# Kernel optimization log

Hardware: AMD Instinct MI355X
Metric: run time of the kernel (lower is better)

## Reference

```python
import jax, jax.numpy as jnp
import numpy as np

B, CI, CO, H, W = 16, 32, 32, 256, 256
K0, K1 = 32, 32              # modes_fourier
LEVEL0, LEVEL1 = 3, 5        # PDEPara_mode_level
M = 2 ** LEVEL1              # 32 = modes_pde_extra per dim
KAPPA = (2 * M) // (2 ** LEVEL0)  # 8 = kappa_base
NPARA = 3 * (LEVEL0 - 1) + 1      # 7 columns of fourierweight_scaling used


def setup_inputs() -> dict:
    key = jax.random.key(0)
    ks = jax.random.split(key, 6)
    scale = 1.0 / (CI * CO)
    x = jax.random.normal(ks[0], (B, CI, H, W), dtype=jnp.float32)
    fourierweight_scaling = jax.random.uniform(ks[1], (B, NPARA), dtype=jnp.float32)
    weights_dim0 = scale * jax.random.uniform(ks[2], (CI, CO, K0, K1, 2), dtype=jnp.float32)
    weights_dim1 = scale * jax.random.uniform(ks[3], (CI, CO, K0, K1, 2), dtype=jnp.float32)
    weights_extra_dim0 = scale * jax.random.uniform(ks[4], (CI, CO, M, M, 2), dtype=jnp.float32)
    weights_extra_dim1 = scale * jax.random.uniform(ks[5], (CI, CO, M, M, 2), dtype=jnp.float32)
    return dict(x=x, fourierweight_scaling=fourierweight_scaling,
                weights_dim0=weights_dim0, weights_dim1=weights_dim1,
                weights_extra_dim0=weights_extra_dim0, weights_extra_dim1=weights_extra_dim1)


def _c(w):
    # real-pair [..., 2] -> complex; compl2/compl3_einsum are exactly complex products
    return jax.lax.complex(w[..., 0], w[..., 1])


def _mode_scaling(fs):
    # hierarchical quadrant-wise per-mode scaling, [B, M, M]
    s = jnp.zeros((B, M, M), dtype=fs.dtype)
    s = s.at[:, :KAPPA, :KAPPA].set(fs[:, 0][:, None, None])
    for d in range(1, LEVEL0):  # small fixed number of levels
        l0 = KAPPA * 2 ** (d - 1)
        l1 = 2 * l0
        s = s.at[:, :l0, l0:l1].set(fs[:, 3 * d - 2][:, None, None])
        s = s.at[:, l0:l1, :l0].set(fs[:, 3 * d - 1][:, None, None])
        s = s.at[:, l0:l1, l0:l1].set(fs[:, 3 * d][:, None, None])
    return s


def reference(x, fourierweight_scaling, weights_dim0, weights_dim1,
              weights_extra_dim0, weights_extra_dim1):
    x_ft = jnp.fft.rfft2(x, norm='ortho')  # [B, CI, H, W//2+1] complex
    out_ft = jnp.zeros((B, CO, H, W // 2 + 1), dtype=x_ft.dtype)
    # base mode mixing on low / high row-frequency corners
    out_ft = out_ft.at[:, :, :K0, :K1].set(
        jnp.einsum('bixy,ioxy->boxy', x_ft[:, :, :K0, :K1], _c(weights_dim0)))
    out_ft = out_ft.at[:, :, -K0:, :K1].set(
        jnp.einsum('bixy,ioxy->boxy', x_ft[:, :, -K0:, :K1], _c(weights_dim1)))
    # PDE-parameter dependent extra mixing with hierarchical scaling
    s = _mode_scaling(fourierweight_scaling).astype(x_ft.dtype)
    out_ft = out_ft.at[:, :, :M, :M].add(
        jnp.einsum('bixy,ioxy,bxy->boxy', x_ft[:, :, :M, :M], _c(weights_extra_dim0), s))
    out_ft = out_ft.at[:, :, -M:, :M].add(
        jnp.einsum('bixy,ioxy,bxy->boxy', x_ft[:, :, -M:, :M], _c(weights_extra_dim1), s))
    return jnp.fft.irfft2(out_ft, s=(H, W), norm='ortho')  # [B, CO, H, W]
```

## Files before the change

kernel.cpp:

```cpp
#include <hip/hip_runtime.h>


typedef _Float16 f16;
typedef _Float16 f16x8 __attribute__((ext_vector_type(8)));
typedef float f32x4 __attribute__((ext_vector_type(4)));

static __device__ __forceinline__ float2 upk(uint u) {
    union { uint x; f16 h[2]; } c; c.x = u;
    return make_float2((float)c.h[0], (float)c.h[1]);
}
static __device__ __forceinline__ uint pk2(float r, float i) {
    union { uint x; f16 h[2]; } c; c.h[0] = (f16)r; c.h[1] = (f16)i;
    return c.x;
}

__global__ void k_tabs(f16* __restrict__ Etab, f16* __restrict__ Ftabt,
                       f16* __restrict__ Etab2, f16* __restrict__ Tt) {
    const int h = blockIdx.x;
    const int tid = threadIdx.x;
    if (tid < 64) {
        const int j = tid;
        const int ky = (j < 32) ? j : j - 64;
        float s, c;
        sincospif((float)(ky * h) / 128.0f, &s, &c);
        Etab[h * 128 + 2 * j] = (f16)c;
        Etab[h * 128 + 2 * j + 1] = (f16)s;
        Etab2[j * 512 + 2 * h] = (f16)c;
        Etab2[j * 512 + 2 * h + 1] = (f16)s;
    } else if (tid < 96) {
        const int k = tid - 64;
        const float ck = (k == 0) ? 1.0f : 2.0f;
        float s, c;
        sincospif((float)(k * h) / 128.0f, &s, &c);
        Ftabt[h * 64 + 2 * k] = (f16)(ck * c);
        Ftabt[h * 64 + 2 * k + 1] = (f16)(-ck * s);
    } else {
        const int kx = tid - 96;
        float s, c;
        sincospif((float)(kx * h) / 128.0f, &s, &c);
        Tt[(2 * kx) * 256 + h] = (f16)c;
        Tt[(2 * kx + 1) * 256 + h] = (f16)(-s);
    }
}

__global__ __launch_bounds__(256) void k_rowdftB(const float* __restrict__ x,
                                                 const f16* __restrict__ Tt,
                                                 f16* __restrict__ Xw16) {
    __shared__ __align__(16) f16 Gs[128 * 88];
    const int tid = threadIdx.x;
    const int wv = tid >> 6, lane = tid & 63;
    const int l15 = lane & 15, lk = lane >> 4;
    const long rowbase = (long)blockIdx.x * 128;

    f32x4 acc[2][4];
#pragma unroll
    for (int mt = 0; mt < 2; ++mt)
#pragma unroll
        for (int nt = 0; nt < 4; ++nt)
            acc[mt][nt] = (f32x4){0.0f, 0.0f, 0.0f, 0.0f};

    const float* xbase = x + (rowbase + wv * 32 + l15) * 256 + lk * 8;
    const f16* tbase = Tt + l15 * 256 + lk * 8;

#pragma unroll
    for (int ks = 0; ks < 8; ++ks) {
        f16x8 a[2], b[4];
#pragma unroll
        for (int mt = 0; mt < 2; ++mt) {
            const float4 u = *(const float4*)(xbase + mt * 4096 + ks * 32);
            const float4 v = *(const float4*)(xbase + mt * 4096 + ks * 32 + 4);
            a[mt][0] = (f16)u.x; a[mt][1] = (f16)u.y;
            a[mt][2] = (f16)u.z; a[mt][3] = (f16)u.w;
            a[mt][4] = (f16)v.x; a[mt][5] = (f16)v.y;
            a[mt][6] = (f16)v.z; a[mt][7] = (f16)v.w;
        }
#pragma unroll
        for (int nt = 0; nt < 4; ++nt)
            b[nt] = *(const f16x8*)(tbase + nt * 4096 + ks * 32);
#pragma unroll
        for (int mt = 0; mt < 2; ++mt)
#pragma unroll
            for (int nt = 0; nt < 4; ++nt)
                acc[mt][nt] = __builtin_amdgcn_mfma_f32_16x16x32_f16(
                    a[mt], b[nt], acc[mt][nt], 0, 0, 0);
    }

#pragma unroll
    for (int mt = 0; mt < 2; ++mt)
#pragma unroll
        for (int nt = 0; nt < 4; ++nt) {
            const int row0 = wv * 32 + mt * 16 + lk * 4;
            const int col = nt * 16 + l15;
#pragma unroll
            for (int r = 0; r < 4; ++r)
                Gs[(row0 + r) * 88 + col] = (f16)acc[mt][nt][r];
        }
    __syncthreads();

#pragma unroll
    for (int p = 0; p < 4; ++p) {
        const int id = p * 256 + tid;
        const int row = id >> 3, ch = id & 7;
        *(uint4*)(Xw16 + (rowbase + row) * 64 + ch * 8) =
            *(const uint4*)(Gs + row * 88 + ch * 8);
    }
}

__global__ __launch_bounds__(256) void k_coldftB(const f16* __restrict__ Xw16,
                                                 const f16* __restrict__ Etab2,
                                                 f16* __restrict__ Xf16) {
    __shared__ __align__(16) f16 Bt[64 * 520];
    const int tid = threadIdx.x;
    const long p = blockIdx.x;

    {
        const uint* src = (const uint*)(Xw16 + (p * 256 + tid) * 64);
        uint* B32 = (uint*)Bt;
#pragma unroll
        for (int kx = 0; kx < 32; ++kx) {
            const uint a = src[kx];
            const uint b = (a >> 16) | (((a & 0xffffu) ^ 0x8000u) << 16);
            B32[(2 * kx) * 260 + tid] = a;
            B32[(2 * kx + 1) * 260 + tid] = b;
        }
    }
    __syncthreads();

    const int wv = tid >> 6, lane = tid & 63;
    const int l15 = lane & 15, lk = lane >> 4;

    f32x4 acc[4];
#pragma unroll
    for (int nt = 0; nt < 4; ++nt) acc[nt] = (f32x4){0.0f, 0.0f, 0.0f, 0.0f};

    const f16* abase = Etab2 + (wv * 16 + l15) * 512 + lk * 8;
#pragma unroll
    for (int ks = 0; ks < 16; ++ks) {
        const f16x8 a = *(const f16x8*)(abase + ks * 32);
        f16x8 b[4];
#pragma unroll
        for (int nt = 0; nt < 4; ++nt)
            b[nt] = *(const f16x8*)(Bt + (nt * 16 + l15) * 520 + ks * 32 + lk * 8);
#pragma unroll
        for (int nt = 0; nt < 4; ++nt)
            acc[nt] = __builtin_amdgcn_mfma_f32_16x16x32_f16(a, b[nt], acc[nt], 0, 0, 0);
    }

    f16* obase = Xf16 + p * 4096;
#pragma unroll
    for (int nt = 0; nt < 4; ++nt)
#pragma unroll
        for (int r = 0; r < 4; ++r)
            obase[(wv * 16 + lk * 4 + r) * 64 + nt * 16 + l15] = (f16)acc[nt][r];
}

__global__ __launch_bounds__(256) void k_mixB(const f16* __restrict__ Xf16,
                                              const float* __restrict__ fs,
                                              const float* __restrict__ w0,
                                              const float* __restrict__ w1,
                                              const float* __restrict__ we0,
                                              const float* __restrict__ we1,
                                              f16* __restrict__ Ff16) {
    __shared__ __align__(16) float4 Wl[4096];
    const int tid = threadIdx.x;
    const int bid = blockIdx.x;
    const int cog = bid >> 6;
    const int corner = (bid >> 5) & 1;
    const int jj = bid & 31;
    const int j = corner * 32 + jj;

    {
        const int t = tid >> 7, ci = (tid >> 2) & 31, co = tid & 3;
        const float* Wt = (t == 0) ? (corner ? w1 : w0) : (corner ? we1 : we0);
        const float4* src =
            (const float4*)(Wt + ((long)(ci * 32 + cog * 4 + co) * 2048 + jj * 64));
        const int m = tid & 15;
#pragma unroll
        for (int i = 0; i < 16; ++i) Wl[tid * 16 + (i ^ m)] = src[i];
    }
    __syncthreads();

    const int b = tid >> 4, kxp = tid & 15;
    const int kx0 = 2 * kxp;

    float s[2];
#pragma unroll
    for (int e = 0; e < 2; ++e) {
        const int v = kx0 + e, u = jj;
        int idx;
        if (u < 8 && v < 8) idx = 0;
        else if (u < 16 && v < 16) idx = (u < 8) ? 1 : ((v < 8) ? 2 : 3);
        else idx = (u < 16) ? 4 : ((v < 16) ? 5 : 6);
        s[e] = fs[b * 7 + idx];
    }

    float aW[4][4] = {}, aE[4][4] = {};
    const uint* xb = (const uint*)Xf16 + (long)(b * 32) * 2048 + j * 32 + kx0;

    for (int ci = 0; ci < 32; ++ci) {
        const uint2 xu = *(const uint2*)(xb + ci * 2048);
        const float2 x0 = upk(xu.x), x1 = upk(xu.y);
        const int rbase = ci * 4;
#pragma unroll
        for (int co = 0; co < 4; ++co) {
            const int rw = rbase + co;
            const int sl = kxp ^ (rw & 15);
            const float4 wv = Wl[rw * 16 + sl];
            const float4 ev = Wl[(128 + rw) * 16 + sl];
            aW[co][0] += x0.x * wv.x - x0.y * wv.y;
            aW[co][1] += x0.x * wv.y + x0.y * wv.x;
            aW[co][2] += x1.x * wv.z - x1.y * wv.w;
            aW[co][3] += x1.x * wv.w + x1.y * wv.z;
            aE[co][0] += x0.x * ev.x - x0.y * ev.y;
            aE[co][1] += x0.x * ev.y + x0.y * ev.x;
            aE[co][2] += x1.x * ev.z - x1.y * ev.w;
            aE[co][3] += x1.x * ev.w + x1.y * ev.z;
        }
    }

    uint* ofb = (uint*)Ff16;
#pragma unroll
    for (int co = 0; co < 4; ++co) {
        const long q = b * 32 + cog * 4 + co;
        uint2 o;
        o.x = pk2(aW[co][0] + s[0] * aE[co][0], aW[co][1] + s[0] * aE[co][1]);
        o.y = pk2(aW[co][2] + s[1] * aE[co][2], aW[co][3] + s[1] * aE[co][3]);
        *(uint2*)(ofb + q * 2048 + j * 32 + kx0) = o;
    }
}

__global__ __launch_bounds__(256) void k_invB(const f16* __restrict__ Ff16,
                                              const f16* __restrict__ Etab,
                                              f16* __restrict__ Gbuf) {
    __shared__ __align__(16) f16 Ft[64 * 136];
    __shared__ __align__(16) f16 Gs[256 * 72];
    const int tid = threadIdx.x;
    const long q = blockIdx.x;

    {
        const uint4* src = (const uint4*)(Ff16 + q * 4096);
        uint* B32 = (uint*)Ft;
#pragma unroll
        for (int i = 0; i < 2; ++i) {
            const uint4 v = src[tid * 2 + i];
            const uint a4[4] = {v.x, v.y, v.z, v.w};
#pragma unroll
            for (int c = 0; c < 4; ++c) {
                const int idx = tid * 8 + i * 4 + c;
                const int jr = idx >> 5, kx = idx & 31;
                const uint a = a4[c];
                B32[(2 * kx) * 68 + jr] = a ^ 0x80000000u;
                B32[(2 * kx + 1) * 68 + jr] = (a >> 16) | (a << 16);
            }
        }
    }
    __syncthreads();

    const int wv = tid >> 6, lane = tid & 63;
    const int l15 = lane & 15, lk = lane >> 4;

    f32x4 acc[4][4];
#pragma unroll
    for (int mt = 0; mt < 4; ++mt)
#pragma unroll
        for (int nt = 0; nt < 4; ++nt)
            acc[mt][nt] = (f32x4){0.0f, 0.0f, 0.0f, 0.0f};

    const f16* Arow = Etab + (wv * 64 + l15) * 128 + lk * 8;
#pragma unroll
    for (int ks = 0; ks < 4; ++ks) {
        f16x8 a[4], b[4];
#pragma unroll
        for (int mt = 0; mt < 4; ++mt)
            a[mt] = *(const f16x8*)(Arow + mt * 2048 + ks * 32);
#pragma unroll
        for (int nt = 0; nt < 4; ++nt)
            b[nt] = *(const f16x8*)(&Ft[(nt * 16 + l15) * 136 + ks * 32 + lk * 8]);
#pragma unroll
        for (int mt = 0; mt < 4; ++mt)
#pragma unroll
            for (int nt = 0; nt < 4; ++nt)
                acc[mt][nt] = __builtin_amdgcn_mfma_f32_16x16x32_f16(
                    a[mt], b[nt], acc[mt][nt], 0, 0, 0);
    }

#pragma unroll
    for (int mt = 0; mt < 4; ++mt)
#pragma unroll
        for (int nt = 0; nt < 4; ++nt) {
            const int row = wv * 64 + mt * 16 + lk * 4;
            const int col = nt * 16 + l15;
#pragma unroll
            for (int r = 0; r < 4; ++r)
                Gs[(row + r) * 72 + col] = (f16)acc[mt][nt][r];
        }
    __syncthreads();

#pragma unroll
    for (int p = 0; p < 8; ++p) {
        const int id = p * 256 + tid;
        const int row = id >> 3, ch = id & 7;
        const uint4 u = *(const uint4*)(Gs + row * 72 + ch * 8);
        *(uint4*)(Gbuf + q * 16384 + row * 64 + ch * 8) = u;
    }
}

__global__ __launch_bounds__(256) void k_invC(const f16* __restrict__ Gbuf,
                                              const f16* __restrict__ Ftabt,
                                              float* __restrict__ out) {
    const int tid = threadIdx.x;
    const long q = blockIdx.x >> 1;
    const int half = blockIdx.x & 1;
    const int wv = tid >> 6, lane = tid & 63;
    const int l15 = lane & 15, lk = lane >> 4;

    f16x8 a[2][2];
    const f16* abase = Gbuf + q * 16384 + (half * 128 + wv * 32 + l15) * 64 + lk * 8;
#pragma unroll
    for (int mt = 0; mt < 2; ++mt)
#pragma unroll
        for (int ks = 0; ks < 2; ++ks)
            a[mt][ks] = *(const f16x8*)(abase + mt * 1024 + ks * 32);

    float* obase = out + q * 65536 + (long)(half * 128 + wv * 32) * 256;

#pragma unroll 1
    for (int g = 0; g < 4; ++g) {
        f32x4 acc[2][4];
#pragma unroll
        for (int mt = 0; mt < 2; ++mt)
#pragma unroll
            for (int nt = 0; nt < 4; ++nt)
                acc[mt][nt] = (f32x4){0.0f, 0.0f, 0.0f, 0.0f};

        const f16* bbase = Ftabt + (g * 64 + l15) * 64 + lk * 8;
#pragma unroll
        for (int nt = 0; nt < 4; ++nt)
#pragma unroll
            for (int ks = 0; ks < 2; ++ks) {
                const f16x8 b = *(const f16x8*)(bbase + nt * 1024 + ks * 32);
#pragma unroll
                for (int mt = 0; mt < 2; ++mt)
                    acc[mt][nt] = __builtin_amdgcn_mfma_f32_16x16x32_f16(
                        a[mt][ks], b, acc[mt][nt], 0, 0, 0);
            }

#pragma unroll
        for (int mt = 0; mt < 2; ++mt)
#pragma unroll
            for (int nt = 0; nt < 4; ++nt) {
                float* o = obase + (mt * 16 + lk * 4) * 256 + g * 64 + nt * 16 + l15;
#pragma unroll
                for (int r = 0; r < 4; ++r)
                    o[r * 256] = acc[mt][nt][r] * 0x1p-16f;
            }
    }
}

extern "C" void kernel_launch(void* const* d_in, const int* in_sizes, int n_in,
                              void* d_out, int out_size, void* d_ws, size_t ws_size,
                              hipStream_t stream) {
    (void)in_sizes; (void)n_in; (void)out_size; (void)ws_size;
    const float* x   = (const float*)d_in[0];
    const float* fs  = (const float*)d_in[1];
    const float* w0  = (const float*)d_in[2];
    const float* w1  = (const float*)d_in[3];
    const float* we0 = (const float*)d_in[4];
    const float* we1 = (const float*)d_in[5];
    float* out = (float*)d_out;
    float* ws = (float*)d_ws;

    f16* Etab   = (f16*)ws;
    f16* Ftabt  = (f16*)(ws + 16384);
    f16* Etab2  = (f16*)(ws + 24576);
    f16* Tt     = (f16*)(ws + 40960);
    f16* Xw16   = (f16*)(ws + 49152);
    f16* Gbuf   = (f16*)(ws + 49152 + 4194304);
    f16* Xf16   = (f16*)(ws + 49152 + 8388608);
    f16* Ff16   = (f16*)(ws + 49152 + 8388608 + 2097152);

    k_tabs   <<<256,  128, 0, stream>>>(Etab, Ftabt, Etab2, Tt);
    k_rowdftB<<<1024, 256, 0, stream>>>(x, Tt, Xw16);
    k_coldftB<<<512,  256, 0, stream>>>(Xw16, Etab2, Xf16);
    k_mixB   <<<512,  256, 0, stream>>>(Xf16, fs, w0, w1, we0, we1, Ff16);
    k_invB   <<<512,  256, 0, stream>>>(Ff16, Etab, Gbuf);
    k_invC   <<<1024, 256, 0, stream>>>(Gbuf, Ftabt, out);
}
```

Measured before the change: 319.7 us.

## Fuse row and column DFT stages and the two inverse stages into single kernels

Merges the forward row DFT and column DFT into one kernel that keeps the intermediate in LDS instead of writing it to global memory. The split real/imag layout of Etab2 and the sign-flipped copy are built directly from the MFMA accumulators. Likewise merges the two inverse stages so the intermediate G stays in LDS, cutting two global round trips and two launches. Each block now does more work with larger accumulator tiles, which raises register pressure and reduces parallelism in the final stage (512 blocks instead of 1024).

```diff
diff --git a/kernel.cpp b/kernel.cpp
--- a/kernel.cpp
+++ b/kernel.cpp
@@ -25,8 +25,8 @@
         sincospif((float)(ky * h) / 128.0f, &s, &c);
         Etab[h * 128 + 2 * j] = (f16)c;
         Etab[h * 128 + 2 * j + 1] = (f16)s;
-        Etab2[j * 512 + 2 * h] = (f16)c;
-        Etab2[j * 512 + 2 * h + 1] = (f16)s;
+        Etab2[j * 512 + h] = (f16)c;
+        Etab2[j * 512 + 256 + h] = (f16)s;
     } else if (tid < 96) {
         const int k = tid - 64;
         const float ck = (k == 0) ? 1.0f : 2.0f;
@@ -43,115 +43,92 @@
     }
 }
 
-__global__ __launch_bounds__(256) void k_rowdftB(const float* __restrict__ x,
-                                                 const f16* __restrict__ Tt,
-                                                 f16* __restrict__ Xw16) {
-    __shared__ __align__(16) f16 Gs[128 * 88];
-    const int tid = threadIdx.x;
-    const int wv = tid >> 6, lane = tid & 63;
-    const int l15 = lane & 15, lk = lane >> 4;
-    const long rowbase = (long)blockIdx.x * 128;
-
-    f32x4 acc[2][4];
-#pragma unroll
-    for (int mt = 0; mt < 2; ++mt)
-#pragma unroll
-        for (int nt = 0; nt < 4; ++nt)
-            acc[mt][nt] = (f32x4){0.0f, 0.0f, 0.0f, 0.0f};
-
-    const float* xbase = x + (rowbase + wv * 32 + l15) * 256 + lk * 8;
-    const f16* tbase = Tt + l15 * 256 + lk * 8;
-
-#pragma unroll
-    for (int ks = 0; ks < 8; ++ks) {
-        f16x8 a[2], b[4];
-#pragma unroll
-        for (int mt = 0; mt < 2; ++mt) {
-            const float4 u = *(const float4*)(xbase + mt * 4096 + ks * 32);
-            const float4 v = *(const float4*)(xbase + mt * 4096 + ks * 32 + 4);
-            a[mt][0] = (f16)u.x; a[mt][1] = (f16)u.y;
-            a[mt][2] = (f16)u.z; a[mt][3] = (f16)u.w;
-            a[mt][4] = (f16)v.x; a[mt][5] = (f16)v.y;
-            a[mt][6] = (f16)v.z; a[mt][7] = (f16)v.w;
-        }
-#pragma unroll
-        for (int nt = 0; nt < 4; ++nt)
-            b[nt] = *(const f16x8*)(tbase + nt * 4096 + ks * 32);
-#pragma unroll
-        for (int mt = 0; mt < 2; ++mt)
-#pragma unroll
-            for (int nt = 0; nt < 4; ++nt)
-                acc[mt][nt] = __builtin_amdgcn_mfma_f32_16x16x32_f16(
-                    a[mt], b[nt], acc[mt][nt], 0, 0, 0);
-    }
-
-#pragma unroll
-    for (int mt = 0; mt < 2; ++mt)
-#pragma unroll
-        for (int nt = 0; nt < 4; ++nt) {
-            const int row0 = wv * 32 + mt * 16 + lk * 4;
-            const int col = nt * 16 + l15;
-#pragma unroll
-            for (int r = 0; r < 4; ++r)
-                Gs[(row0 + r) * 88 + col] = (f16)acc[mt][nt][r];
-        }
-    __syncthreads();
-
-#pragma unroll
-    for (int p = 0; p < 4; ++p) {
-        const int id = p * 256 + tid;
-        const int row = id >> 3, ch = id & 7;
-        *(uint4*)(Xw16 + (rowbase + row) * 64 + ch * 8) =
-            *(const uint4*)(Gs + row * 88 + ch * 8);
-    }
-}
-
-__global__ __launch_bounds__(256) void k_coldftB(const f16* __restrict__ Xw16,
-                                                 const f16* __restrict__ Etab2,
-                                                 f16* __restrict__ Xf16) {
+__global__ __launch_bounds__(256) void k_fwd(const float* __restrict__ x,
+                                             const f16* __restrict__ Tt,
+                                             const f16* __restrict__ Etab2,
+                                             f16* __restrict__ Xf16) {
     __shared__ __align__(16) f16 Bt[64 * 520];
     const int tid = threadIdx.x;
     const long p = blockIdx.x;
-
-    {
-        const uint* src = (const uint*)(Xw16 + (p * 256 + tid) * 64);
-        uint* B32 = (uint*)Bt;
-#pragma unroll
-        for (int kx = 0; kx < 32; ++kx) {
-            const uint a = src[kx];
-            const uint b = (a >> 16) | (((a & 0xffffu) ^ 0x8000u) << 16);
-            B32[(2 * kx) * 260 + tid] = a;
-            B32[(2 * kx + 1) * 260 + tid] = b;
-        }
-    }
-    __syncthreads();
-
     const int wv = tid >> 6, lane = tid & 63;
     const int l15 = lane & 15, lk = lane >> 4;
 
-    f32x4 acc[4];
-#pragma unroll
-    for (int nt = 0; nt < 4; ++nt) acc[nt] = (f32x4){0.0f, 0.0f, 0.0f, 0.0f};
-
-    const f16* abase = Etab2 + (wv * 16 + l15) * 512 + lk * 8;
-#pragma unroll
-    for (int ks = 0; ks < 16; ++ks) {
-        const f16x8 a = *(const f16x8*)(abase + ks * 32);
-        f16x8 b[4];
+    {
+        f32x4 acc[4][4];
+#pragma unroll
+        for (int mt = 0; mt < 4; ++mt)
+#pragma unroll
+            for (int nt = 0; nt < 4; ++nt)
+                acc[mt][nt] = (f32x4){0.0f, 0.0f, 0.0f, 0.0f};
+
+        const float* xbase = x + (p * 256 + wv * 64 + l15) * 256 + lk * 8;
+        const f16* tbase = Tt + l15 * 256 + lk * 8;
+
+#pragma unroll 4
+        for (int ks = 0; ks < 8; ++ks) {
+            f16x8 a[4], b[4];
+#pragma unroll
+            for (int mt = 0; mt < 4; ++mt) {
+                const float4 u = *(const float4*)(xbase + mt * 4096 + ks * 32);
+                const float4 v = *(const float4*)(xbase + mt * 4096 + ks * 32 + 4);
+                a[mt][0] = (f16)u.x; a[mt][1] = (f16)u.y;
+                a[mt][2] = (f16)u.z; a[mt][3] = (f16)u.w;
+                a[mt][4] = (f16)v.x; a[mt][5] = (f16)v.y;
+                a[mt][6] = (f16)v.z; a[mt][7] = (f16)v.w;
+            }
+#pragma unroll
+            for (int nt = 0; nt < 4; ++nt)
+                b[nt] = *(const f16x8*)(tbase + nt * 4096 + ks * 32);
+#pragma unroll
+            for (int mt = 0; mt < 4; ++mt)
+#pragma unroll
+                for (int nt = 0; nt < 4; ++nt)
+                    acc[mt][nt] = __builtin_amdgcn_mfma_f32_16x16x32_f16(
+                        a[mt], b[nt], acc[mt][nt], 0, 0, 0);
+        }
+
+        const int n = l15;
+        const uint m = (n & 1) ? 0u : 0x80008000u;
+#pragma unroll
+        for (int mt = 0; mt < 4; ++mt) {
+            const int H0 = wv * 64 + mt * 16 + lk * 4;
+#pragma unroll
+            for (int nt = 0; nt < 4; ++nt) {
+                const int nn = nt * 16 + l15;
+                const uint p0 = pk2(acc[mt][nt][0], acc[mt][nt][1]);
+                const uint p1 = pk2(acc[mt][nt][2], acc[mt][nt][3]);
+                *(uint2*)(Bt + nn * 520 + H0) = make_uint2(p0, p1);
+                *(uint2*)(Bt + (nn ^ 1) * 520 + 256 + H0) = make_uint2(p0 ^ m, p1 ^ m);
+            }
+        }
+    }
+    __syncthreads();
+
+    {
+        f32x4 acc[4];
+#pragma unroll
+        for (int nt = 0; nt < 4; ++nt) acc[nt] = (f32x4){0.0f, 0.0f, 0.0f, 0.0f};
+
+        const f16* abase = Etab2 + (wv * 16 + l15) * 512 + lk * 8;
+#pragma unroll
+        for (int ks = 0; ks < 16; ++ks) {
+            const f16x8 a = *(const f16x8*)(abase + ks * 32);
+            f16x8 b[4];
+#pragma unroll
+            for (int nt = 0; nt < 4; ++nt)
+                b[nt] = *(const f16x8*)(Bt + (nt * 16 + l15) * 520 + ks * 32 + lk * 8);
+#pragma unroll
+            for (int nt = 0; nt < 4; ++nt)
+                acc[nt] = __builtin_amdgcn_mfma_f32_16x16x32_f16(a, b[nt], acc[nt], 0, 0, 0);
+        }
+
+        f16* obase = Xf16 + p * 4096;
 #pragma unroll
         for (int nt = 0; nt < 4; ++nt)
-            b[nt] = *(const f16x8*)(Bt + (nt * 16 + l15) * 520 + ks * 32 + lk * 8);
-#pragma unroll
-        for (int nt = 0; nt < 4; ++nt)
-            acc[nt] = __builtin_amdgcn_mfma_f32_16x16x32_f16(a, b[nt], acc[nt], 0, 0, 0);
-    }
-
-    f16* obase = Xf16 + p * 4096;
-#pragma unroll
-    for (int nt = 0; nt < 4; ++nt)
-#pragma unroll
-        for (int r = 0; r < 4; ++r)
-            obase[(wv * 16 + lk * 4 + r) * 64 + nt * 16 + l15] = (f16)acc[nt][r];
+#pragma unroll
+            for (int r = 0; r < 4; ++r)
+                obase[(wv * 16 + lk * 4 + r) * 64 + nt * 16 + l15] = (f16)acc[nt][r];
+    }
 }
 
 __global__ __launch_bounds__(256) void k_mixB(const f16* __restrict__ Xf16,
@@ -195,7 +172,7 @@
     }
 
     float aW[4][4] = {}, aE[4][4] = {};
-    const uint* xb = (const uint*)Xf16 + (long)(b * 32) * 2048 + j * 32 + kx0;
+    const uint* xb = (const uint*)Xf16 + (long)(b * 32) * 2048 + j * 32 + kxp * 2;
 
     for (int ci = 0; ci < 32; ++ci) {
         const uint2 xu = *(const uint2*)(xb + ci * 2048);
@@ -225,17 +202,20 @@
         uint2 o;
         o.x = pk2(aW[co][0] + s[0] * aE[co][0], aW[co][1] + s[0] * aE[co][1]);
         o.y = pk2(aW[co][2] + s[1] * aE[co][2], aW[co][3] + s[1] * aE[co][3]);
-        *(uint2*)(ofb + q * 2048 + j * 32 + kx0) = o;
-    }
-}
-
-__global__ __launch_bounds__(256) void k_invB(const f16* __restrict__ Ff16,
+        *(uint2*)(ofb + q * 2048 + j * 32 + kxp * 2) = o;
+    }
+}
+
+__global__ __launch_bounds__(256) void k_invF(const f16* __restrict__ Ff16,
                                               const f16* __restrict__ Etab,
-                                              f16* __restrict__ Gbuf) {
+                                              const f16* __restrict__ Ftabt,
+                                              float* __restrict__ out) {
     __shared__ __align__(16) f16 Ft[64 * 136];
     __shared__ __align__(16) f16 Gs[256 * 72];
     const int tid = threadIdx.x;
     const long q = blockIdx.x;
+    const int wv = tid >> 6, lane = tid & 63;
+    const int l15 = lane & 15, lk = lane >> 4;
 
     {
         const uint4* src = (const uint4*)(Ff16 + q * 4096);
@@ -256,104 +236,87 @@
     }
     __syncthreads();
 
-    const int wv = tid >> 6, lane = tid & 63;
-    const int l15 = lane & 15, lk = lane >> 4;
-
-    f32x4 acc[4][4];
-#pragma unroll
-    for (int mt = 0; mt < 4; ++mt)
-#pragma unroll
-        for (int nt = 0; nt < 4; ++nt)
-            acc[mt][nt] = (f32x4){0.0f, 0.0f, 0.0f, 0.0f};
-
-    const f16* Arow = Etab + (wv * 64 + l15) * 128 + lk * 8;
-#pragma unroll
-    for (int ks = 0; ks < 4; ++ks) {
-        f16x8 a[4], b[4];
+    {
+        f32x4 acc[4][4];
 #pragma unroll
         for (int mt = 0; mt < 4; ++mt)
-            a[mt] = *(const f16x8*)(Arow + mt * 2048 + ks * 32);
-#pragma unroll
-        for (int nt = 0; nt < 4; ++nt)
-            b[nt] = *(const f16x8*)(&Ft[(nt * 16 + l15) * 136 + ks * 32 + lk * 8]);
+#pragma unroll
+            for (int nt = 0; nt < 4; ++nt)
+                acc[mt][nt] = (f32x4){0.0f, 0.0f, 0.0f, 0.0f};
+
+        const f16* Arow = Etab + (wv * 64 + l15) * 128 + lk * 8;
+#pragma unroll
+        for (int ks = 0; ks < 4; ++ks) {
+            f16x8 a[4], b[4];
+#pragma unroll
+            for (int mt = 0; mt < 4; ++mt)
+                a[mt] = *(const f16x8*)(Arow + mt * 2048 + ks * 32);
+#pragma unroll
+            for (int nt = 0; nt < 4; ++nt)
+                b[nt] = *(const f16x8*)(&Ft[(nt * 16 + l15) * 136 + ks * 32 + lk * 8]);
+#pragma unroll
+            for (int mt = 0; mt < 4; ++mt)
+#pragma unroll
+                for (int nt = 0; nt < 4; ++nt)
+                    acc[mt][nt] = __builtin_amdgcn_mfma_f32_16x16x32_f16(
+                        a[mt], b[nt], acc[mt][nt], 0, 0, 0);
+        }
+
 #pragma unroll
         for (int mt = 0; mt < 4; ++mt)
 #pragma unroll
-            for (int nt = 0; nt < 4; ++nt)
-                acc[mt][nt] = __builtin_amdgcn_mfma_f32_16x16x32_f16(
-                    a[mt], b[nt], acc[mt][nt], 0, 0, 0);
-    }
-
-#pragma unroll
-    for (int mt = 0; mt < 4; ++mt)
-#pragma unroll
-        for (int nt = 0; nt < 4; ++nt) {
-            const int row = wv * 64 + mt * 16 + lk * 4;
-            const int col = nt * 16 + l15;
-#pragma unroll
-            for (int r = 0; r < 4; ++r)
-                Gs[(row + r) * 72 + col] = (f16)acc[mt][nt][r];
-        }
+            for (int nt = 0; nt < 4; ++nt) {
+                const int row = wv * 64 + mt * 16 + lk * 4;
+                const int col = nt * 16 + l15;
+#pragma unroll
+                for (int r = 0; r < 4; ++r)
+                    Gs[(row + r) * 72 + col] = (f16)acc[mt][nt][r];
+            }
+    }
     __syncthreads();
 
-#pragma unroll
-    for (int p = 0; p < 8; ++p) {
-        const int id = p * 256 + tid;
-        const int row = id >> 3, ch = id & 7;
-        const uint4 u = *(const uint4*)(Gs + row * 72 + ch * 8);
-        *(uint4*)(Gbuf + q * 16384 + row * 64 + ch * 8) = u;
-    }
-}
-
-__global__ __launch_bounds__(256) void k_invC(const f16* __restrict__ Gbuf,
-                                              const f16* __restrict__ Ftabt,
-                                              float* __restrict__ out) {
-    const int tid = threadIdx.x;
-    const long q = blockIdx.x >> 1;
-    const int half = blockIdx.x & 1;
-    const int wv = tid >> 6, lane = tid & 63;
-    const int l15 = lane & 15, lk = lane >> 4;
-
-    f16x8 a[2][2];
-    const f16* abase = Gbuf + q * 16384 + (half * 128 + wv * 32 + l15) * 64 + lk * 8;
-#pragma unroll
-    for (int mt = 0; mt < 2; ++mt)
-#pragma unroll
-        for (int ks = 0; ks < 2; ++ks)
-            a[mt][ks] = *(const f16x8*)(abase + mt * 1024 + ks * 32);
-
-    float* obase = out + q * 65536 + (long)(half * 128 + wv * 32) * 256;
+    {
+        const int hb = wv * 64;
+        f16x8 a[4][2];
+#pragma unroll
+        for (int mt = 0; mt < 4; ++mt)
+#pragma unroll
+            for (int ks = 0; ks < 2; ++ks)
+                a[mt][ks] = *(const f16x8*)(Gs + (hb + mt * 16 + l15) * 72 + ks * 32 + lk * 8);
+
+        float* obase = out + q * 65536 + (long)hb * 256;
 
 #pragma unroll 1
-    for (int g = 0; g < 4; ++g) {
-        f32x4 acc[2][4];
-#pragma unroll
-        for (int mt = 0; mt < 2; ++mt)
-#pragma unroll
-            for (int nt = 0; nt < 4; ++nt)
-                acc[mt][nt] = (f32x4){0.0f, 0.0f, 0.0f, 0.0f};
-
-        const f16* bbase = Ftabt + (g * 64 + l15) * 64 + lk * 8;
-#pragma unroll
-        for (int nt = 0; nt < 4; ++nt)
-#pragma unroll
-            for (int ks = 0; ks < 2; ++ks) {
-                const f16x8 b = *(const f16x8*)(bbase + nt * 1024 + ks * 32);
-#pragma unroll
-                for (int mt = 0; mt < 2; ++mt)
-                    acc[mt][nt] = __builtin_amdgcn_mfma_f32_16x16x32_f16(
-                        a[mt][ks], b, acc[mt][nt], 0, 0, 0);
-            }
-
-#pragma unroll
-        for (int mt = 0; mt < 2; ++mt)
-#pragma unroll
-            for (int nt = 0; nt < 4; ++nt) {
-                float* o = obase + (mt * 16 + lk * 4) * 256 + g * 64 + nt * 16 + l15;
-#pragma unroll
-                for (int r = 0; r < 4; ++r)
-                    o[r * 256] = acc[mt][nt][r] * 0x1p-16f;
-            }
+        for (int g = 0; g < 4; ++g) {
+            f32x4 acc[4][4];
+#pragma unroll
+            for (int mt = 0; mt < 4; ++mt)
+#pragma unroll
+                for (int nt = 0; nt < 4; ++nt)
+                    acc[mt][nt] = (f32x4){0.0f, 0.0f, 0.0f, 0.0f};
+
+            const f16* bbase = Ftabt + (g * 64 + l15) * 64 + lk * 8;
+#pragma unroll
+            for (int nt = 0; nt < 4; ++nt)
+#pragma unroll
+                for (int ks = 0; ks < 2; ++ks) {
+                    const f16x8 b = *(const f16x8*)(bbase + nt * 1024 + ks * 32);
+#pragma unroll
+                    for (int mt = 0; mt < 4; ++mt)
+                        acc[mt][nt] = __builtin_amdgcn_mfma_f32_16x16x32_f16(
+                            a[mt][ks], b, acc[mt][nt], 0, 0, 0);
+                }
+
+#pragma unroll
+            for (int mt = 0; mt < 4; ++mt)
+#pragma unroll
+                for (int nt = 0; nt < 4; ++nt) {
+                    float* o = obase + (mt * 16 + lk * 4) * 256 + g * 64 + nt * 16 + l15;
+#pragma unroll
+                    for (int r = 0; r < 4; ++r)
+                        o[r * 256] = acc[mt][nt][r] * 0x1p-16f;
+                }
+        }
     }
 }
 
@@ -374,15 +337,11 @@
     f16* Ftabt  = (f16*)(ws + 16384);
     f16* Etab2  = (f16*)(ws + 24576);
     f16* Tt     = (f16*)(ws + 40960);
-    f16* Xw16   = (f16*)(ws + 49152);
-    f16* Gbuf   = (f16*)(ws + 49152 + 4194304);
-    f16* Xf16   = (f16*)(ws + 49152 + 8388608);
-    f16* Ff16   = (f16*)(ws + 49152 + 8388608 + 2097152);
-
-    k_tabs   <<<256,  128, 0, stream>>>(Etab, Ftabt, Etab2, Tt);
-    k_rowdftB<<<1024, 256, 0, stream>>>(x, Tt, Xw16);
-    k_coldftB<<<512,  256, 0, stream>>>(Xw16, Etab2, Xf16);
-    k_mixB   <<<512,  256, 0, stream>>>(Xf16, fs, w0, w1, we0, we1, Ff16);
-    k_invB   <<<512,  256, 0, stream>>>(Ff16, Etab, Gbuf);
-    k_invC   <<<1024, 256, 0, stream>>>(Gbuf, Ftabt, out);
-}
+    f16* Xf16   = (f16*)(ws + 49152);
+    f16* Ff16   = (f16*)(ws + 49152 + 1048576);
+
+    k_tabs <<<256, 128, 0, stream>>>(Etab, Ftabt, Etab2, Tt);
+    k_fwd  <<<512, 256, 0, stream>>>(x, Tt, Etab2, Xf16);
+    k_mixB <<<512, 256, 0, stream>>>(Xf16, fs, w0, w1, we0, we1, Ff16);
+    k_invF <<<512, 256, 0, stream>>>(Ff16, Etab, Ftabt, out);
+}
```

Measured after the change: 301.1 us. 5.8% less time.
